# Kernel tuning notes

Hardware: AMD Instinct MI355X
Metric: run time of the kernel (lower is better)

The kernel has to match this reference:

```python
import jax, jax.numpy as jnp
import numpy as np

GROUP_SIZE = 128
LORA_ALPHA = 32
R = 16
SCALING = LORA_ALPHA / R  # lora_alpha / r


def setup_inputs() -> dict:
    key = jax.random.key(0)
    k1, k2, k3, k4, k5, k6 = jax.random.split(key, 6)
    B, S, IN, OUT = 8, 16, 4096, 11008
    G = IN // GROUP_SIZE  # 32 quantization groups
    x = jax.random.normal(k1, (B, S, IN), dtype=jnp.float32)
    int_weight = jax.random.randint(k2, (IN, OUT), 0, 16, dtype=jnp.int32)  # int4 codes
    zeros = jax.random.randint(k3, (G, OUT), 0, 16, dtype=jnp.int32)        # per-group zero points
    scales = jax.random.uniform(k4, (G, OUT), dtype=jnp.float32) * 0.02     # per-group scales
    lora_A = jax.random.normal(k5, (R, IN), dtype=jnp.float32) * (1.0 / np.sqrt(IN))
    lora_B = jax.random.normal(k6, (OUT, R), dtype=jnp.float32) * 0.02
    return {"x": x, "int_weight": int_weight, "zeros": zeros,
            "scales": scales, "lora_A": lora_A, "lora_B": lora_B}


def reference(x, int_weight, zeros, scales, lora_A, lora_B):
    # Dequantize int4 weights: w[i, o] = (q[i, o] - zero[g(i), o]) * scale[g(i), o]
    zeros_f = jnp.repeat(zeros.astype(jnp.float32), GROUP_SIZE, axis=0)   # [IN, OUT]
    scales_f = jnp.repeat(scales, GROUP_SIZE, axis=0)                     # [IN, OUT]
    w = (int_weight.astype(jnp.float32) - zeros_f) * scales_f             # [IN, OUT]
    # qlinear: x @ W_deq
    base = jnp.einsum('bsi,io->bso', x, w)
    # LoRA: x @ A^T @ B^T * scaling  (dropout=0 -> identity)
    lora = jnp.einsum('bsr,or->bso', jnp.einsum('bsi,ri->bsr', x, lora_A), lora_B)
    return base + lora * SCALING
```

## Files before the change

### kernel.cpp

```cpp
#include <hip/hip_runtime.h>
#include <hip/hip_bf16.h>

typedef __bf16 bf16_t;
typedef __bf16 bf16x8 __attribute__((ext_vector_type(8)));
typedef __bf16 bf16x4 __attribute__((ext_vector_type(4)));
typedef float f32x4 __attribute__((ext_vector_type(4)));

#define M_TOK 128
#define K_IN 4096
#define N_OUT 11008
#define R_LORA 16
#define SCALING 2.0f

__global__ __launch_bounds__(256) void k_prep(const float* __restrict__ x,
                                              const float* __restrict__ loraA,
                                              float* __restrict__ T,
                                              bf16_t* __restrict__ xb) {
  const int m = blockIdx.x;
  __shared__ float xs[K_IN];
  const float4* xr = (const float4*)(x + (size_t)m * K_IN);
  bf16x4* xbr = (bf16x4*)(xb + (size_t)m * K_IN);
  for (int i = threadIdx.x; i < K_IN / 4; i += 256) {
    float4 v = xr[i];
    ((float4*)xs)[i] = v;
    bf16x4 pv = {(bf16_t)v.x, (bf16_t)v.y, (bf16_t)v.z, (bf16_t)v.w};
    xbr[i] = pv;
  }
  __syncthreads();
  const int w = threadIdx.x >> 6;
  const int lane = threadIdx.x & 63;
  float a0 = 0.f, a1 = 0.f, a2 = 0.f, a3 = 0.f;
  const float4* A0 = (const float4*)(loraA + (size_t)(w * 4 + 0) * K_IN);
  const float4* A1 = (const float4*)(loraA + (size_t)(w * 4 + 1) * K_IN);
  const float4* A2 = (const float4*)(loraA + (size_t)(w * 4 + 2) * K_IN);
  const float4* A3 = (const float4*)(loraA + (size_t)(w * 4 + 3) * K_IN);
  for (int i = lane; i < K_IN / 4; i += 64) {
    float4 xv = ((float4*)xs)[i];
    float4 v0 = A0[i], v1 = A1[i], v2 = A2[i], v3 = A3[i];
    a0 += xv.x * v0.x + xv.y * v0.y + xv.z * v0.z + xv.w * v0.w;
    a1 += xv.x * v1.x + xv.y * v1.y + xv.z * v1.z + xv.w * v1.w;
    a2 += xv.x * v2.x + xv.y * v2.y + xv.z * v2.z + xv.w * v2.w;
    a3 += xv.x * v3.x + xv.y * v3.y + xv.z * v3.z + xv.w * v3.w;
  }
#pragma unroll
  for (int off = 32; off; off >>= 1) {
    a0 += __shfl_down(a0, off);
    a1 += __shfl_down(a1, off);
    a2 += __shfl_down(a2, off);
    a3 += __shfl_down(a3, off);
  }
  if (lane == 0) {
    float* tm = T + m * R_LORA + w * 4;
    tm[0] = a0 * SCALING;
    tm[1] = a1 * SCALING;
    tm[2] = a2 * SCALING;
    tm[3] = a3 * SCALING;
  }
}

__global__ __launch_bounds__(256) void k_lora(const float* __restrict__ T,
                                              const float* __restrict__ loraB,
                                              float* __restrict__ out) {
  const int b = blockIdx.x;
  const int m = b / 43;
  const int o = (b % 43) * 256 + threadIdx.x;
  const float* t = T + m * R_LORA;
  const float4* br = (const float4*)(loraB + (size_t)o * R_LORA);
  float4 b0 = br[0], b1 = br[1], b2 = br[2], b3 = br[3];
  float s = t[0] * b0.x + t[1] * b0.y + t[2] * b0.z + t[3] * b0.w +
            t[4] * b1.x + t[5] * b1.y + t[6] * b1.z + t[7] * b1.w +
            t[8] * b2.x + t[9] * b2.y + t[10] * b2.z + t[11] * b2.w +
            t[12] * b3.x + t[13] * b3.y + t[14] * b3.z + t[15] * b3.w;
  out[(size_t)m * N_OUT + o] = s;
}

#define NSTRIPS 172
#define WSTRIDE 56

__global__ __launch_bounds__(256) void k_main(const int* __restrict__ qw,
                                              const int* __restrict__ zr,
                                              const float* __restrict__ sc,
                                              const bf16_t* __restrict__ xb,
                                              float* __restrict__ out) {
  const int nb = blockIdx.x % NSTRIPS;
  const int kc = blockIdx.x / NSTRIPS;
  const int o0 = nb * 64;
  const int k0 = kc * 1024;

  __shared__ __align__(16) bf16_t wlds[2][64 * WSTRIDE];

  const int tid = threadIdx.x;
  const int w = tid >> 6;
  const int lane = tid & 63;

  const int oq = tid & 63;
  const int kq = w * 8;
  const int ocol = o0 + oq;
  const int* qp = qw + (size_t)(k0 + kq) * N_OUT + ocol;

  float sf, nzs;
  {
    const int g0 = k0 >> 7;
    float s_ = sc[(size_t)g0 * N_OUT + ocol];
    int z_ = zr[(size_t)g0 * N_OUT + ocol];
    sf = s_;
    nzs = -(float)z_ * s_;
  }

  int qr[8];
#pragma unroll
  for (int j = 0; j < 8; ++j) qr[j] = qp[(size_t)j * N_OUT];
  {
    bf16x8 wv;
#pragma unroll
    for (int j = 0; j < 8; ++j) wv[j] = (bf16_t)fmaf((float)qr[j], sf, nzs);
    *(bf16x8*)&wlds[0][oq * WSTRIDE + kq] = wv;
  }

  f32x4 acc[2][4];
#pragma unroll
  for (int mt = 0; mt < 2; ++mt)
#pragma unroll
    for (int ot = 0; ot < 4; ++ot) acc[mt][ot] = (f32x4){0.f, 0.f, 0.f, 0.f};

  const int aq = (lane >> 4) * 8;
  const bf16_t* ap = xb + (size_t)(w * 32 + (lane & 15)) * K_IN + k0 + aq;

  for (int step = 0; step < 32; ++step) {
    __syncthreads();
    const int buf = step & 1;

    if (step + 1 < 32) {
      const int* qn = qp + (size_t)(step + 1) * 32 * N_OUT;
#pragma unroll
      for (int j = 0; j < 8; ++j) qr[j] = qn[(size_t)j * N_OUT];
      if (((step + 1) & 3) == 0) {
        const int g = (k0 >> 7) + ((step + 1) >> 2);
        float s_ = sc[(size_t)g * N_OUT + ocol];
        int z_ = zr[(size_t)g * N_OUT + ocol];
        sf = s_;
        nzs = -(float)z_ * s_;
      }
    }

    bf16x8 a0 = *(const bf16x8*)(ap + step * 32);
    bf16x8 a1 = *(const bf16x8*)(ap + (size_t)16 * K_IN + step * 32);

#pragma unroll
    for (int ot = 0; ot < 4; ++ot) {
      bf16x8 bfrag = *(bf16x8*)&wlds[buf][(ot * 16 + (lane & 15)) * WSTRIDE + aq];
      acc[0][ot] = __builtin_amdgcn_mfma_f32_16x16x32_bf16(a0, bfrag, acc[0][ot], 0, 0, 0);
      acc[1][ot] = __builtin_amdgcn_mfma_f32_16x16x32_bf16(a1, bfrag, acc[1][ot], 0, 0, 0);
    }

    if (step + 1 < 32) {
      bf16x8 wv;
#pragma unroll
      for (int j = 0; j < 8; ++j) wv[j] = (bf16_t)fmaf((float)qr[j], sf, nzs);
      *(bf16x8*)&wlds[1 - buf][oq * WSTRIDE + kq] = wv;
    }
  }

#pragma unroll
  for (int mt = 0; mt < 2; ++mt) {
    const int m = w * 32 + mt * 16 + ((lane >> 4) << 2);
#pragma unroll
    for (int ot = 0; ot < 4; ++ot) {
      const int o = o0 + ot * 16 + (lane & 15);
#pragma unroll
      for (int r = 0; r < 4; ++r)
        unsafeAtomicAdd(&out[(size_t)(m + r) * N_OUT + o], acc[mt][ot][r]);
    }
  }
}

extern "C" void kernel_launch(void* const* d_in, const int* in_sizes, int n_in,
                              void* d_out, int out_size, void* d_ws, size_t ws_size,
                              hipStream_t stream) {
  const float* x = (const float*)d_in[0];
  const int* qw = (const int*)d_in[1];
  const int* zr = (const int*)d_in[2];
  const float* sc = (const float*)d_in[3];
  const float* loraA = (const float*)d_in[4];
  const float* loraB = (const float*)d_in[5];
  float* out = (float*)d_out;

  float* T = (float*)d_ws;
  bf16_t* xb = (bf16_t*)((char*)d_ws + 8192);

  k_prep<<<dim3(M_TOK), dim3(256), 0, stream>>>(x, loraA, T, xb);
  k_lora<<<dim3(M_TOK * 43), dim3(256), 0, stream>>>(T, loraB, out);
  k_main<<<dim3(NSTRIPS * 4), dim3(256), 0, stream>>>(qw, zr, sc, xb, out);
}
```

Measured before the change: 298.6 us.

## Double K-step depth, preload all group scales, fully unroll main loop

```diff
diff --git a/kernel.cpp b/kernel.cpp
--- a/kernel.cpp
+++ b/kernel.cpp
@@ -75,13 +75,13 @@
 }
 
 #define NSTRIPS 172
-#define WSTRIDE 56
-
-__global__ __launch_bounds__(256) void k_main(const int* __restrict__ qw,
-                                              const int* __restrict__ zr,
-                                              const float* __restrict__ sc,
-                                              const bf16_t* __restrict__ xb,
-                                              float* __restrict__ out) {
+#define WSTRIDE 72
+
+__global__ __launch_bounds__(256, 4) void k_main(const int* __restrict__ qw,
+                                                 const int* __restrict__ zr,
+                                                 const float* __restrict__ sc,
+                                                 const bf16_t* __restrict__ xb,
+                                                 float* __restrict__ out) {
   const int nb = blockIdx.x % NSTRIPS;
   const int kc = blockIdx.x / NSTRIPS;
   const int o0 = nb * 64;
@@ -92,29 +92,35 @@
   const int tid = threadIdx.x;
   const int w = tid >> 6;
   const int lane = tid & 63;
-
-  const int oq = tid & 63;
-  const int kq = w * 8;
+  const int oq = lane;
+  const int kq = w * 16;
   const int ocol = o0 + oq;
   const int* qp = qw + (size_t)(k0 + kq) * N_OUT + ocol;
 
-  float sf, nzs;
+  float sf[8], nzs[8];
   {
     const int g0 = k0 >> 7;
-    float s_ = sc[(size_t)g0 * N_OUT + ocol];
-    int z_ = zr[(size_t)g0 * N_OUT + ocol];
-    sf = s_;
-    nzs = -(float)z_ * s_;
-  }
-
-  int qr[8];
-#pragma unroll
-  for (int j = 0; j < 8; ++j) qr[j] = qp[(size_t)j * N_OUT];
+#pragma unroll
+    for (int g = 0; g < 8; ++g) {
+      float s_ = sc[(size_t)(g0 + g) * N_OUT + ocol];
+      int z_ = zr[(size_t)(g0 + g) * N_OUT + ocol];
+      sf[g] = s_;
+      nzs[g] = -(float)z_ * s_;
+    }
+  }
+
+  int qr[16];
+#pragma unroll
+  for (int j = 0; j < 16; ++j) qr[j] = qp[(size_t)j * N_OUT];
   {
-    bf16x8 wv;
-#pragma unroll
-    for (int j = 0; j < 8; ++j) wv[j] = (bf16_t)fmaf((float)qr[j], sf, nzs);
-    *(bf16x8*)&wlds[0][oq * WSTRIDE + kq] = wv;
+    bf16x8 wv0, wv1;
+#pragma unroll
+    for (int j = 0; j < 8; ++j) {
+      wv0[j] = (bf16_t)fmaf((float)qr[j], sf[0], nzs[0]);
+      wv1[j] = (bf16_t)fmaf((float)qr[8 + j], sf[0], nzs[0]);
+    }
+    *(bf16x8*)&wlds[0][oq * WSTRIDE + kq] = wv0;
+    *(bf16x8*)&wlds[0][oq * WSTRIDE + kq + 8] = wv1;
   }
 
   f32x4 acc[2][4];
@@ -126,38 +132,40 @@
   const int aq = (lane >> 4) * 8;
   const bf16_t* ap = xb + (size_t)(w * 32 + (lane & 15)) * K_IN + k0 + aq;
 
-  for (int step = 0; step < 32; ++step) {
+#pragma unroll
+  for (int step = 0; step < 16; ++step) {
     __syncthreads();
     const int buf = step & 1;
 
-    if (step + 1 < 32) {
-      const int* qn = qp + (size_t)(step + 1) * 32 * N_OUT;
-#pragma unroll
-      for (int j = 0; j < 8; ++j) qr[j] = qn[(size_t)j * N_OUT];
-      if (((step + 1) & 3) == 0) {
-        const int g = (k0 >> 7) + ((step + 1) >> 2);
-        float s_ = sc[(size_t)g * N_OUT + ocol];
-        int z_ = zr[(size_t)g * N_OUT + ocol];
-        sf = s_;
-        nzs = -(float)z_ * s_;
+    if (step + 1 < 16) {
+      const int* qn = qp + (size_t)(step + 1) * 64 * N_OUT;
+#pragma unroll
+      for (int j = 0; j < 16; ++j) qr[j] = qn[(size_t)j * N_OUT];
+    }
+
+#pragma unroll
+    for (int ks = 0; ks < 2; ++ks) {
+      bf16x8 a0 = *(const bf16x8*)(ap + step * 64 + ks * 32);
+      bf16x8 a1 = *(const bf16x8*)(ap + (size_t)16 * K_IN + step * 64 + ks * 32);
+#pragma unroll
+      for (int ot = 0; ot < 4; ++ot) {
+        bf16x8 bfrag =
+            *(bf16x8*)&wlds[buf][(ot * 16 + (lane & 15)) * WSTRIDE + ks * 32 + aq];
+        acc[0][ot] = __builtin_amdgcn_mfma_f32_16x16x32_bf16(a0, bfrag, acc[0][ot], 0, 0, 0);
+        acc[1][ot] = __builtin_amdgcn_mfma_f32_16x16x32_bf16(a1, bfrag, acc[1][ot], 0, 0, 0);
       }
     }
 
-    bf16x8 a0 = *(const bf16x8*)(ap + step * 32);
-    bf16x8 a1 = *(const bf16x8*)(ap + (size_t)16 * K_IN + step * 32);
-
-#pragma unroll
-    for (int ot = 0; ot < 4; ++ot) {
-      bf16x8 bfrag = *(bf16x8*)&wlds[buf][(ot * 16 + (lane & 15)) * WSTRIDE + aq];
-      acc[0][ot] = __builtin_amdgcn_mfma_f32_16x16x32_bf16(a0, bfrag, acc[0][ot], 0, 0, 0);
-      acc[1][ot] = __builtin_amdgcn_mfma_f32_16x16x32_bf16(a1, bfrag, acc[1][ot], 0, 0, 0);
-    }
-
-    if (step + 1 < 32) {
-      bf16x8 wv;
-#pragma unroll
-      for (int j = 0; j < 8; ++j) wv[j] = (bf16_t)fmaf((float)qr[j], sf, nzs);
-      *(bf16x8*)&wlds[1 - buf][oq * WSTRIDE + kq] = wv;
+    if (step + 1 < 16) {
+      const int g = (step + 1) >> 1;
+      bf16x8 wv0, wv1;
+#pragma unroll
+      for (int j = 0; j < 8; ++j) {
+        wv0[j] = (bf16_t)fmaf((float)qr[j], sf[g], nzs[g]);
+        wv1[j] = (bf16_t)fmaf((float)qr[8 + j], sf[g], nzs[g]);
+      }
+      *(bf16x8*)&wlds[1 - buf][oq * WSTRIDE + kq] = wv0;
+      *(bf16x8*)&wlds[1 - buf][oq * WSTRIDE + kq + 8] = wv1;
     }
   }
 
```

After: 293.6 us. About the same (-1.7%).
